# Performance work log

Measured on AMD Instinct MI355X. Metric: run time of the kernel, lower is better.

## Reference

```python
import jax, jax.numpy as jnp
import numpy as np

N = 100000      # nodes
E = 3200000     # edges (avg degree 32)
F_IN = 500      # PubMed node features
H = 16          # hidden
C = 3           # PubMed classes


def setup_inputs() -> dict:
    key = jax.random.key(0)
    k1, k2, k3, k4, k5, k6 = jax.random.split(key, 6)
    x = jax.random.normal(k1, (N, F_IN), dtype=jnp.float32)
    edge_index = jax.random.randint(k2, (2, E), 0, N, dtype=jnp.int32)
    # GCNConv weights (glorot-ish scale) and zero biases
    W1 = jax.random.normal(k3, (F_IN, H), dtype=jnp.float32) * np.float32(np.sqrt(2.0 / (F_IN + H)))
    b1 = jnp.zeros((H,), dtype=jnp.float32)
    W2 = jax.random.normal(k4, (H, C), dtype=jnp.float32) * np.float32(np.sqrt(2.0 / (H + C)))
    b2 = jnp.zeros((C,), dtype=jnp.float32)
    return {"x": x, "W1": W1, "b1": b1, "W2": W2, "b2": b2, "edge_index": edge_index}


def gcn_layer(x, W, b, src, dst, n):
    # GCNConv: linear transform, add self-loops, symmetric degree normalization, scatter-add
    h = x @ W                                   # [N, F_out]
    loop = jnp.arange(n, dtype=src.dtype)
    s = jnp.concatenate([src, loop])            # [E+N]
    d = jnp.concatenate([dst, loop])            # [E+N]
    deg = jax.ops.segment_sum(jnp.ones_like(d, dtype=h.dtype), d, num_segments=n)
    dinv = jax.lax.rsqrt(jnp.maximum(deg, 1.0))  # deg >= 1 due to self-loops
    norm = dinv[s] * dinv[d]                    # [E+N]
    out = jax.ops.segment_sum(h[s] * norm[:, None], d, num_segments=n)
    return out + b


def reference(x, W1, b1, W2, b2, edge_index):
    src, dst = edge_index[0], edge_index[1]
    h = gcn_layer(x, W1, b1, src, dst, N)
    h = jax.nn.relu(h)
    # F.dropout in eval mode (reference is deterministic) is identity
    out = gcn_layer(h, W2, b2, src, dst, N)
    return jax.nn.log_softmax(out, axis=1)
```

## Files before the change

### kernel.cpp

```cpp
#include <hip/hip_runtime.h>
#include <hip/hip_fp16.h>
#include <math.h>

#define N_NODES 100000
#define N_EDGES 3200000
#define F_INF   500
#define H_DIM   16
#define C_DIM   3

#define NB      782
#define CAP     4608
#define GPAD    16
#define EPB     16384
#define NBLK_PART ((N_EDGES + EPB - 1) / EPB)

#define OFF_GCUR  0
#define OFF_DINV  12512
#define OFF_PAIRS 112512
#define OFF_ROWS  3715968
#define OFF_H1H   3816064
#define OFF_H2H   4616064

typedef float        f32x4 __attribute__((ext_vector_type(4)));
typedef unsigned int u32x4 __attribute__((ext_vector_type(4)));
typedef unsigned int u32x2 __attribute__((ext_vector_type(2)));

template <typename T>
__device__ inline T ntload(const T* p) { return __builtin_nontemporal_load(p); }
template <typename T>
__device__ inline void ntstore(T* p, T v) { __builtin_nontemporal_store(v, p); }

__device__ inline float2 h2f(unsigned u) {
    __half2 h = *reinterpret_cast<__half2*>(&u);
    return __half22float2(h);
}
__device__ inline unsigned f2h(float a, float b) {
    __half2 h = __floats2half2_rn(a, b);
    return *reinterpret_cast<unsigned*>(&h);
}

__global__ void k_init(int* __restrict__ gcur) {
    int b = blockIdx.x * 256 + threadIdx.x;
    if (b < NB) gcur[b * GPAD] = b * CAP;
}

__global__ __launch_bounds__(512) void k_part(const int* __restrict__ src,
                                              const int* __restrict__ dst,
                                              int* __restrict__ gcur,
                                              unsigned int* __restrict__ pairs) {
    __shared__ unsigned sbuf[EPB];
    __shared__ int lcnt[NB];
    __shared__ int lbase[NB];
    __shared__ int lstart[NB];
    __shared__ int lrank[NB];
    __shared__ int wtot[8];
    int t = threadIdx.x;
    int wid = t >> 6, lane = t & 63;
    int e0 = blockIdx.x * EPB;
    for (int i = t; i < NB; i += 512) { lcnt[i] = 0; lrank[i] = 0; }
    __syncthreads();
    for (int i = t; i < EPB; i += 512) {
        int e = e0 + i;
        if (e < N_EDGES) atomicAdd(&lcnt[ntload(dst + e) >> 7], 1);
    }
    __syncthreads();
    for (int b = t; b < NB; b += 512) {
        int c = lcnt[b];
        lbase[b] = c ? atomicAdd(&gcur[b * GPAD], c) : 0;
    }
    {
        int b0 = wid * 128 + lane * 2;
        int c0 = (b0 < NB) ? lcnt[b0] : 0;
        int c1 = (b0 + 1 < NB) ? lcnt[b0 + 1] : 0;
        int s = c0 + c1;
        int inc = s;
        for (int o = 1; o < 64; o <<= 1) { int y = __shfl_up(inc, o); if (lane >= o) inc += y; }
        if (lane == 63) wtot[wid] = inc;
        int excl = inc - s;
        if (b0 < NB) lstart[b0] = excl;
        if (b0 + 1 < NB) lstart[b0 + 1] = excl + c0;
    }
    __syncthreads();
    if (t == 0) { int r = 0; for (int w = 0; w < 8; ++w) { int v = wtot[w]; wtot[w] = r; r += v; } }
    __syncthreads();
    {
        int b0 = wid * 128 + lane * 2;
        int add = wtot[wid];
        if (b0 < NB) lstart[b0] += add;
        if (b0 + 1 < NB) lstart[b0 + 1] += add;
    }
    __syncthreads();
    for (int i = t; i < EPB; i += 512) {
        int e = e0 + i;
        if (e < N_EDGES) {
            int d = ntload(dst + e);
            int b = d >> 7;
            int r = atomicAdd(&lrank[b], 1);
            sbuf[lstart[b] + r] = ((unsigned)ntload(src + e) << 7) | (unsigned)(d & 127);
        }
    }
    __syncthreads();
    for (int b = wid; b < NB; b += 8) {
        int c = lcnt[b], ls = lstart[b], gb = lbase[b];
        int lim = (b + 1) * CAP;
        for (int i = lane; i < c; i += 64) {
            int pos = gb + i;
            if (pos < lim)
                pairs[pos] = sbuf[ls + i];
        }
    }
}

__global__ __launch_bounds__(512) void k_sort(unsigned int* __restrict__ pairs,
                                              const int* __restrict__ gcur,
                                              float* __restrict__ dinv,
                                              int* __restrict__ rows) {
    __shared__ unsigned sbuf[CAP];
    __shared__ unsigned sout[CAP];
    __shared__ int cnt[128];
    __shared__ int start[128];
    __shared__ int rank[128];
    int b = blockIdx.x, t = threadIdx.x;
    if (t < 128) { cnt[t] = 0; rank[t] = 0; }
    __syncthreads();
    int base = b * CAP;
    int n = min(gcur[b * GPAD] - base, CAP);
    for (int i = t; i < n; i += 512) {
        unsigned p = ntload(pairs + base + i);
        sbuf[i] = p;
        atomicAdd(&cnt[p & 127], 1);
    }
    __syncthreads();
    if (t < 64) {
        int c0 = cnt[2 * t], c1 = cnt[2 * t + 1];
        int s = c0 + c1;
        int inc = s;
        for (int o = 1; o < 64; o <<= 1) { int y = __shfl_up(inc, o); if (t >= o) inc += y; }
        int excl = inc - s;
        start[2 * t] = excl;
        start[2 * t + 1] = excl + c0;
        rows[b * 128 + 2 * t]     = (excl << 16) | c0;
        rows[b * 128 + 2 * t + 1] = ((excl + c0) << 16) | c1;
    }
    if (t >= 64 && t < 192) {
        int l = t - 64;
        int v = b * 128 + l;
        if (v < N_NODES) dinv[v] = rsqrtf((float)(cnt[l] + 1));
    }
    __syncthreads();
    for (int i = t; i < n; i += 512) {
        unsigned p = sbuf[i];
        int k = p & 127;
        int r = atomicAdd(&rank[k], 1);
        sout[start[k] + r] = p;
    }
    __syncthreads();
    for (int i = t; i < n; i += 512) ntstore(pairs + base + i, sout[i]);
}

#define KTILE 16
#define KSTRIDE 17
#define GROWS 128
#define NFULL 31
#define KTAIL 4
#define NTILE 32
__global__ __launch_bounds__(128, 8) void k_gemm1(const float* __restrict__ x,
                                                  const float* __restrict__ W1,
                                                  const float* __restrict__ dinv,
                                                  unsigned int* __restrict__ h1h) {
    __shared__ float xs[GROWS * KSTRIDE];
    int t = threadIdx.x;
    int row0 = blockIdx.x * GROWS;
    int row = row0 + t;
    int cc = t & 3;
    int rr = t >> 2;
    float acc[16];
#pragma unroll
    for (int j = 0; j < 16; ++j) acc[j] = 0.f;
    f32x4 vreg[4];
#pragma unroll
    for (int s = 0; s < 4; ++s) {
        int gr = row0 + s * 32 + rr;
        if (gr < N_NODES)
            vreg[s] = ntload(reinterpret_cast<const f32x4*>(x + (size_t)gr * F_INF + cc * 4));
    }
#pragma unroll 1
    for (int tile = 0; tile < NTILE; ++tile) {
        int k0 = tile * KTILE;
        int nchunks = (tile < NFULL) ? 4 : 1;
        __syncthreads();
#pragma unroll
        for (int s = 0; s < 4; ++s) {
            int r = s * 32 + rr;
            if (cc < nchunks && row0 + r < N_NODES) {
                float* q = xs + r * KSTRIDE + cc * 4;
                q[0] = vreg[s].x; q[1] = vreg[s].y; q[2] = vreg[s].z; q[3] = vreg[s].w;
            }
        }
        __syncthreads();
        if (tile < NTILE - 1) {
            int nk0 = k0 + KTILE;
            int nnc = (tile + 1 < NFULL) ? 4 : 1;
#pragma unroll
            for (int s = 0; s < 4; ++s) {
                int gr = row0 + s * 32 + rr;
                if (cc < nnc && gr < N_NODES)
                    vreg[s] = ntload(reinterpret_cast<const f32x4*>(x + (size_t)gr * F_INF + nk0 + cc * 4));
            }
        }
        if (row < N_NODES) {
            const float* xrow = xs + t * KSTRIDE;
            const float* Wt = W1 + k0 * 16;
            if (tile < NFULL) {
#pragma unroll
                for (int kk = 0; kk < KTILE; ++kk) {
                    float xv = xrow[kk];
#pragma unroll
                    for (int j = 0; j < 16; ++j) acc[j] = fmaf(xv, Wt[kk * 16 + j], acc[j]);
                }
            } else {
#pragma unroll
                for (int kk = 0; kk < KTAIL; ++kk) {
                    float xv = xrow[kk];
#pragma unroll
                    for (int j = 0; j < 16; ++j) acc[j] = fmaf(xv, Wt[kk * 16 + j], acc[j]);
                }
            }
        }
    }
    if (row < N_NODES) {
        float dv = dinv[row];
        u32x4 o0, o1;
        o0.x = f2h(dv * acc[0],  dv * acc[1]);  o0.y = f2h(dv * acc[2],  dv * acc[3]);
        o0.z = f2h(dv * acc[4],  dv * acc[5]);  o0.w = f2h(dv * acc[6],  dv * acc[7]);
        o1.x = f2h(dv * acc[8],  dv * acc[9]);  o1.y = f2h(dv * acc[10], dv * acc[11]);
        o1.z = f2h(dv * acc[12], dv * acc[13]); o1.w = f2h(dv * acc[14], dv * acc[15]);
        u32x4* o = reinterpret_cast<u32x4*>(h1h + (size_t)row * 8);
        ntstore(o, o0);
        ntstore(o + 1, o1);
    }
}

__global__ __launch_bounds__(512) void k_agg1(const unsigned int* __restrict__ pairs,
                                              const int* __restrict__ rows,
                                              const float* __restrict__ dinv,
                                              const unsigned int* __restrict__ h1h,
                                              const float* __restrict__ b1,
                                              const float* __restrict__ W2,
                                              unsigned int* __restrict__ h2h) {
    int b = blockIdx.x, t = threadIdx.x;
    int q = t & 3;
    int l = t >> 2;
    int v = b * 128 + l;
    if (v >= N_NODES) return;
    int e = rows[b * 128 + l];
    int st = b * CAP + (e >> 16);
    int cnt = e & 0xffff;
    int qo = q * 2;
    float dv = dinv[v];
    float s0 = 0.f, s1 = 0.f, s2 = 0.f, s3 = 0.f;
    int i = 0;
    for (; i + 8 <= cnt; i += 8) {
        unsigned p[8];
#pragma unroll
        for (int u = 0; u < 8; ++u) p[u] = ntload(pairs + st + i + u);
        u32x2 A[8];
#pragma unroll
        for (int u = 0; u < 8; ++u)
            A[u] = *reinterpret_cast<const u32x2*>(h1h + (size_t)(p[u] >> 7) * 8 + qo);
#pragma unroll
        for (int u = 0; u < 8; ++u) {
            float2 f0 = h2f(A[u].x), f1 = h2f(A[u].y);
            s0 += f0.x; s1 += f0.y; s2 += f1.x; s3 += f1.y;
        }
    }
    for (; i < cnt; ++i) {
        unsigned p = ntload(pairs + st + i);
        u32x2 A = *reinterpret_cast<const u32x2*>(h1h + (size_t)(p >> 7) * 8 + qo);
        float2 f0 = h2f(A.x), f1 = h2f(A.y);
        s0 += f0.x; s1 += f0.y; s2 += f1.x; s3 += f1.y;
    }
    u32x2 S = *reinterpret_cast<const u32x2*>(h1h + (size_t)v * 8 + qo);
    float2 t0 = h2f(S.x), t1 = h2f(S.y);
    f32x4 bb = reinterpret_cast<const f32x4*>(b1)[q];
    float a0 = fmaxf(fmaf(dv, s0 + t0.x, bb.x), 0.f);
    float a1 = fmaxf(fmaf(dv, s1 + t0.y, bb.y), 0.f);
    float a2 = fmaxf(fmaf(dv, s2 + t1.x, bb.z), 0.f);
    float a3 = fmaxf(fmaf(dv, s3 + t1.y, bb.w), 0.f);
    const float* Wq = W2 + q * 4 * 3;
    float c0 = fmaf(a0, Wq[0], fmaf(a1, Wq[3], fmaf(a2, Wq[6],  a3 * Wq[9])));
    float c1 = fmaf(a0, Wq[1], fmaf(a1, Wq[4], fmaf(a2, Wq[7],  a3 * Wq[10])));
    float c2 = fmaf(a0, Wq[2], fmaf(a1, Wq[5], fmaf(a2, Wq[8],  a3 * Wq[11])));
    c0 += __shfl_xor(c0, 1); c0 += __shfl_xor(c0, 2);
    c1 += __shfl_xor(c1, 1); c1 += __shfl_xor(c1, 2);
    c2 += __shfl_xor(c2, 1); c2 += __shfl_xor(c2, 2);
    if (q == 0) {
        u32x2 o;
        o.x = f2h(dv * c0, dv * c1);
        o.y = f2h(dv * c2, 0.f);
        ntstore(reinterpret_cast<u32x2*>(h2h) + v, o);
    }
}

__global__ __launch_bounds__(256) void k_agg2(const unsigned int* __restrict__ pairs,
                                              const int* __restrict__ rows,
                                              const float* __restrict__ dinv,
                                              const unsigned int* __restrict__ h2h,
                                              const float* __restrict__ b2,
                                              float* __restrict__ out) {
    int b = blockIdx.x, t = threadIdx.x;
    int half = t & 1;
    int l = t >> 1;
    int v = b * 128 + l;
    if (v >= N_NODES) return;
    int e = rows[b * 128 + l];
    int st = b * CAP + (e >> 16);
    int cnt = e & 0xffff;
    const u32x2* h2v = reinterpret_cast<const u32x2*>(h2h);
    float c0 = 0.f, c1 = 0.f, c2 = 0.f;
    int i = half;
    for (; i + 6 < cnt; i += 8) {
        unsigned p0 = ntload(pairs + st + i);
        unsigned p1 = ntload(pairs + st + i + 2);
        unsigned p2 = ntload(pairs + st + i + 4);
        unsigned p3 = ntload(pairs + st + i + 6);
        u32x2 A = h2v[p0 >> 7];
        u32x2 B = h2v[p1 >> 7];
        u32x2 C = h2v[p2 >> 7];
        u32x2 D = h2v[p3 >> 7];
        float2 f01, f2_;
        f01 = h2f(A.x); f2_ = h2f(A.y); c0 += f01.x; c1 += f01.y; c2 += f2_.x;
        f01 = h2f(B.x); f2_ = h2f(B.y); c0 += f01.x; c1 += f01.y; c2 += f2_.x;
        f01 = h2f(C.x); f2_ = h2f(C.y); c0 += f01.x; c1 += f01.y; c2 += f2_.x;
        f01 = h2f(D.x); f2_ = h2f(D.y); c0 += f01.x; c1 += f01.y; c2 += f2_.x;
    }
    for (; i < cnt; i += 2) {
        unsigned p = ntload(pairs + st + i);
        u32x2 A = h2v[p >> 7];
        float2 f01 = h2f(A.x), f2_ = h2f(A.y);
        c0 += f01.x; c1 += f01.y; c2 += f2_.x;
    }
    c0 += __shfl_xor(c0, 1);
    c1 += __shfl_xor(c1, 1);
    c2 += __shfl_xor(c2, 1);
    if (half == 0) {
        float dv = dinv[v];
        u32x2 hv = h2v[v];
        float2 f01 = h2f(hv.x), f2_ = h2f(hv.y);
        float z0 = fmaf(dv, c0 + f01.x, b2[0]);
        float z1 = fmaf(dv, c1 + f01.y, b2[1]);
        float z2 = fmaf(dv, c2 + f2_.x, b2[2]);
        float mx = fmaxf(z0, fmaxf(z1, z2));
        float lse = logf(expf(z0 - mx) + expf(z1 - mx) + expf(z2 - mx));
        out[v * 3 + 0] = z0 - mx - lse;
        out[v * 3 + 1] = z1 - mx - lse;
        out[v * 3 + 2] = z2 - mx - lse;
    }
}

extern "C" void kernel_launch(void* const* d_in, const int* in_sizes, int n_in,
                              void* d_out, int out_size, void* d_ws, size_t ws_size,
                              hipStream_t stream) {
    (void)in_sizes; (void)n_in; (void)out_size; (void)ws_size;
    const float* x  = (const float*)d_in[0];
    const float* W1 = (const float*)d_in[1];
    const float* b1 = (const float*)d_in[2];
    const float* W2 = (const float*)d_in[3];
    const float* b2 = (const float*)d_in[4];
    const int*   ei = (const int*)d_in[5];
    const int* src = ei;
    const int* dst = ei + N_EDGES;
    float* out = (float*)d_out;

    int* ws = (int*)d_ws;
    int*          gcur  = ws + OFF_GCUR;
    float*        dinv  = (float*)(ws + OFF_DINV);
    unsigned int* pairs = (unsigned int*)(ws + OFF_PAIRS);
    int*          rows  = ws + OFF_ROWS;
    unsigned int* h1h   = (unsigned int*)(ws + OFF_H1H);
    unsigned int* h2h   = (unsigned int*)(ws + OFF_H2H);

    k_init <<<(NB + 255) / 256, 256, 0, stream>>>(gcur);
    k_part <<<NBLK_PART, 512, 0, stream>>>(src, dst, gcur, pairs);
    k_sort <<<NB, 512, 0, stream>>>(pairs, gcur, dinv, rows);
    k_gemm1<<<NB, GROWS, 0, stream>>>(x, W1, dinv, h1h);
    k_agg1 <<<NB, 512, 0, stream>>>(pairs, rows, dinv, h1h, b1, W2, h2h);
    k_agg2 <<<NB, 256, 0, stream>>>(pairs, rows, dinv, h2h, b2, out);
}
```

Before: 524.9 us.

## Split each GEMM1 row across four threads and stage W1 in LDS

```diff
diff --git a/kernel.cpp b/kernel.cpp
--- a/kernel.cpp
+++ b/kernel.cpp
@@ -159,85 +159,85 @@
 }
 
 #define KTILE 16
-#define KSTRIDE 17
+#define KSTRIDE 20
 #define GROWS 128
 #define NFULL 31
-#define KTAIL 4
 #define NTILE 32
-__global__ __launch_bounds__(128, 8) void k_gemm1(const float* __restrict__ x,
+__global__ __launch_bounds__(512, 6) void k_gemm1(const float* __restrict__ x,
                                                   const float* __restrict__ W1,
                                                   const float* __restrict__ dinv,
                                                   unsigned int* __restrict__ h1h) {
     __shared__ float xs[GROWS * KSTRIDE];
+    __shared__ float wlds[F_INF * 16];
     int t = threadIdx.x;
     int row0 = blockIdx.x * GROWS;
-    int row = row0 + t;
-    int cc = t & 3;
-    int rr = t >> 2;
-    float acc[16];
-#pragma unroll
-    for (int j = 0; j < 16; ++j) acc[j] = 0.f;
-    f32x4 vreg[4];
-#pragma unroll
-    for (int s = 0; s < 4; ++s) {
-        int gr = row0 + s * 32 + rr;
-        if (gr < N_NODES)
-            vreg[s] = ntload(reinterpret_cast<const f32x4*>(x + (size_t)gr * F_INF + cc * 4));
-    }
+    int q = t & 3;
+    int r = t >> 2;
+    int row = row0 + r;
+    bool rowok = row < N_NODES;
+
+    {
+        const f32x4* Wg = reinterpret_cast<const f32x4*>(W1);
+        f32x4* Wl = reinterpret_cast<f32x4*>(wlds);
+        for (int i = t; i < F_INF * 4; i += 512) Wl[i] = ntload(Wg + i);
+    }
+
+    float acc[4] = {0.f, 0.f, 0.f, 0.f};
+    f32x4 vreg;
+    if (rowok)
+        vreg = ntload(reinterpret_cast<const f32x4*>(x + (size_t)row * F_INF + q * 4));
+
 #pragma unroll 1
     for (int tile = 0; tile < NTILE; ++tile) {
         int k0 = tile * KTILE;
-        int nchunks = (tile < NFULL) ? 4 : 1;
         __syncthreads();
-#pragma unroll
-        for (int s = 0; s < 4; ++s) {
-            int r = s * 32 + rr;
-            if (cc < nchunks && row0 + r < N_NODES) {
-                float* q = xs + r * KSTRIDE + cc * 4;
-                q[0] = vreg[s].x; q[1] = vreg[s].y; q[2] = vreg[s].z; q[3] = vreg[s].w;
-            }
+        if (rowok && (tile < NFULL || q == 0)) {
+            float* p = xs + r * KSTRIDE + q * 4;
+            p[0] = vreg.x; p[1] = vreg.y; p[2] = vreg.z; p[3] = vreg.w;
         }
         __syncthreads();
         if (tile < NTILE - 1) {
             int nk0 = k0 + KTILE;
-            int nnc = (tile + 1 < NFULL) ? 4 : 1;
-#pragma unroll
-            for (int s = 0; s < 4; ++s) {
-                int gr = row0 + s * 32 + rr;
-                if (cc < nnc && gr < N_NODES)
-                    vreg[s] = ntload(reinterpret_cast<const f32x4*>(x + (size_t)gr * F_INF + nk0 + cc * 4));
-            }
-        }
-        if (row < N_NODES) {
-            const float* xrow = xs + t * KSTRIDE;
-            const float* Wt = W1 + k0 * 16;
+            if (rowok && (tile + 1 < NFULL || q == 0))
+                vreg = ntload(reinterpret_cast<const f32x4*>(x + (size_t)row * F_INF + nk0 + q * 4));
+        }
+        if (rowok) {
+            const float* xrow = xs + r * KSTRIDE;
+            const float* wq = wlds + k0 * 16 + q * 4;
             if (tile < NFULL) {
 #pragma unroll
-                for (int kk = 0; kk < KTILE; ++kk) {
-                    float xv = xrow[kk];
-#pragma unroll
-                    for (int j = 0; j < 16; ++j) acc[j] = fmaf(xv, Wt[kk * 16 + j], acc[j]);
+                for (int g = 0; g < 4; ++g) {
+                    f32x4 xv = *reinterpret_cast<const f32x4*>(xrow + g * 4);
+#pragma unroll
+                    for (int kk = 0; kk < 4; ++kk) {
+                        f32x4 wv = *reinterpret_cast<const f32x4*>(wq + (g * 4 + kk) * 16);
+                        float xvk = xv[kk];
+                        acc[0] = fmaf(xvk, wv.x, acc[0]);
+                        acc[1] = fmaf(xvk, wv.y, acc[1]);
+                        acc[2] = fmaf(xvk, wv.z, acc[2]);
+                        acc[3] = fmaf(xvk, wv.w, acc[3]);
+                    }
                 }
             } else {
-#pragma unroll
-                for (int kk = 0; kk < KTAIL; ++kk) {
-                    float xv = xrow[kk];
-#pragma unroll
-                    for (int j = 0; j < 16; ++j) acc[j] = fmaf(xv, Wt[kk * 16 + j], acc[j]);
+                f32x4 xv = *reinterpret_cast<const f32x4*>(xrow);
+#pragma unroll
+                for (int kk = 0; kk < 4; ++kk) {
+                    f32x4 wv = *reinterpret_cast<const f32x4*>(wq + kk * 16);
+                    float xvk = xv[kk];
+                    acc[0] = fmaf(xvk, wv.x, acc[0]);
+                    acc[1] = fmaf(xvk, wv.y, acc[1]);
+                    acc[2] = fmaf(xvk, wv.z, acc[2]);
+                    acc[3] = fmaf(xvk, wv.w, acc[3]);
                 }
             }
         }
     }
-    if (row < N_NODES) {
+    if (rowok) {
         float dv = dinv[row];
-        u32x4 o0, o1;
-        o0.x = f2h(dv * acc[0],  dv * acc[1]);  o0.y = f2h(dv * acc[2],  dv * acc[3]);
-        o0.z = f2h(dv * acc[4],  dv * acc[5]);  o0.w = f2h(dv * acc[6],  dv * acc[7]);
-        o1.x = f2h(dv * acc[8],  dv * acc[9]);  o1.y = f2h(dv * acc[10], dv * acc[11]);
-        o1.z = f2h(dv * acc[12], dv * acc[13]); o1.w = f2h(dv * acc[14], dv * acc[15]);
-        u32x4* o = reinterpret_cast<u32x4*>(h1h + (size_t)row * 8);
-        ntstore(o, o0);
-        ntstore(o + 1, o1);
+        u32x2 o;
+        o.x = f2h(dv * acc[0], dv * acc[1]);
+        o.y = f2h(dv * acc[2], dv * acc[3]);
+        ntstore(reinterpret_cast<u32x2*>(h1h + (size_t)row * 8 + q * 2), o);
     }
 }
 
@@ -383,7 +383,7 @@
     k_init <<<(NB + 255) / 256, 256, 0, stream>>>(gcur);
     k_part <<<NBLK_PART, 512, 0, stream>>>(src, dst, gcur, pairs);
     k_sort <<<NB, 512, 0, stream>>>(pairs, gcur, dinv, rows);
-    k_gemm1<<<NB, GROWS, 0, stream>>>(x, W1, dinv, h1h);
+    k_gemm1<<<NB, 512, 0, stream>>>(x, W1, dinv, h1h);
     k_agg1 <<<NB, 512, 0, stream>>>(pairs, rows, dinv, h1h, b1, W2, h2h);
     k_agg2 <<<NB, 256, 0, stream>>>(pairs, rows, dinv, h2h, b2, out);
 }
```

After: 489.5 us. 6.7% less time.

## Split GEMM1 K dimension across four waves with 64-wide tiles and smem reduction

Applied to the files above, without the earlier changes.

```diff
diff --git a/kernel.cpp b/kernel.cpp
--- a/kernel.cpp
+++ b/kernel.cpp
@@ -158,25 +158,29 @@
     for (int i = t; i < n; i += 512) ntstore(pairs + base + i, sout[i]);
 }
 
-#define KTILE 16
-#define KSTRIDE 17
-#define GROWS 128
-#define NFULL 31
-#define KTAIL 4
-#define NTILE 32
-__global__ __launch_bounds__(128, 8) void k_gemm1(const float* __restrict__ x,
+#define GK_ROWS 128
+#define GK_STRIDE 68
+#define GK_ROUNDS 8
+__global__ __launch_bounds__(512, 6) void k_gemm1(const float* __restrict__ x,
                                                   const float* __restrict__ W1,
                                                   const float* __restrict__ dinv,
                                                   unsigned int* __restrict__ h1h) {
-    __shared__ float xs[GROWS * KSTRIDE];
+    __shared__ float smem[GK_ROWS * GK_STRIDE];
     int t = threadIdx.x;
-    int row0 = blockIdx.x * GROWS;
-    int row = row0 + t;
-    int cc = t & 3;
-    int rr = t >> 2;
+    int row0 = blockIdx.x * GK_ROWS;
+    int cc = t & 15;
+    int rr = t >> 4;
+    int lane = t & 63;
+    int wid  = t >> 6;
+    int g    = wid & 3;
+    int crow = (wid >> 2) * 64 + lane;
+    int grow = row0 + crow;
+    bool rowok = grow < N_NODES;
+
     float acc[16];
 #pragma unroll
     for (int j = 0; j < 16; ++j) acc[j] = 0.f;
+
     f32x4 vreg[4];
 #pragma unroll
     for (int s = 0; s < 4; ++s) {
@@ -184,60 +188,90 @@
         if (gr < N_NODES)
             vreg[s] = ntload(reinterpret_cast<const f32x4*>(x + (size_t)gr * F_INF + cc * 4));
     }
+
 #pragma unroll 1
-    for (int tile = 0; tile < NTILE; ++tile) {
-        int k0 = tile * KTILE;
-        int nchunks = (tile < NFULL) ? 4 : 1;
+    for (int rd = 0; rd < GK_ROUNDS; ++rd) {
+        int k0 = rd * 64;
+        int kw = (rd < GK_ROUNDS - 1) ? 64 : (F_INF - 64 * (GK_ROUNDS - 1));
         __syncthreads();
-#pragma unroll
-        for (int s = 0; s < 4; ++s) {
-            int r = s * 32 + rr;
-            if (cc < nchunks && row0 + r < N_NODES) {
-                float* q = xs + r * KSTRIDE + cc * 4;
-                q[0] = vreg[s].x; q[1] = vreg[s].y; q[2] = vreg[s].z; q[3] = vreg[s].w;
+        if (cc * 4 < kw) {
+#pragma unroll
+            for (int s = 0; s < 4; ++s) {
+                int r = s * 32 + rr;
+                if (row0 + r < N_NODES) {
+                    float* p = smem + r * GK_STRIDE + cc * 4;
+                    p[0] = vreg[s].x; p[1] = vreg[s].y; p[2] = vreg[s].z; p[3] = vreg[s].w;
+                }
             }
         }
         __syncthreads();
-        if (tile < NTILE - 1) {
-            int nk0 = k0 + KTILE;
-            int nnc = (tile + 1 < NFULL) ? 4 : 1;
-#pragma unroll
-            for (int s = 0; s < 4; ++s) {
-                int gr = row0 + s * 32 + rr;
-                if (cc < nnc && gr < N_NODES)
-                    vreg[s] = ntload(reinterpret_cast<const f32x4*>(x + (size_t)gr * F_INF + nk0 + cc * 4));
+        if (rd < GK_ROUNDS - 1) {
+            int nk0 = k0 + 64;
+            int nkw = (rd + 1 < GK_ROUNDS - 1) ? 64 : (F_INF - 64 * (GK_ROUNDS - 1));
+            if (cc * 4 < nkw) {
+#pragma unroll
+                for (int s = 0; s < 4; ++s) {
+                    int gr = row0 + s * 32 + rr;
+                    if (gr < N_NODES)
+                        vreg[s] = ntload(reinterpret_cast<const f32x4*>(x + (size_t)gr * F_INF + nk0 + cc * 4));
+                }
             }
         }
-        if (row < N_NODES) {
-            const float* xrow = xs + t * KSTRIDE;
-            const float* Wt = W1 + k0 * 16;
-            if (tile < NFULL) {
-#pragma unroll
-                for (int kk = 0; kk < KTILE; ++kk) {
-                    float xv = xrow[kk];
-#pragma unroll
-                    for (int j = 0; j < 16; ++j) acc[j] = fmaf(xv, Wt[kk * 16 + j], acc[j]);
+        int klen = kw - g * 16; if (klen > 16) klen = 16;
+        if (klen > 0 && rowok) {
+            const float* xr = smem + crow * GK_STRIDE + g * 16;
+            const float* Wu = W1 + (k0 + g * 16) * 16;
+            if (klen == 16) {
+#pragma unroll
+                for (int c4 = 0; c4 < 4; ++c4) {
+                    f32x4 xv = *reinterpret_cast<const f32x4*>(xr + c4 * 4);
+#pragma unroll
+                    for (int kk = 0; kk < 4; ++kk) {
+                        float xvk = xv[kk];
+                        const float* wk = Wu + (c4 * 4 + kk) * 16;
+#pragma unroll
+                        for (int j = 0; j < 16; ++j) acc[j] = fmaf(xvk, wk[j], acc[j]);
+                    }
                 }
             } else {
-#pragma unroll
-                for (int kk = 0; kk < KTAIL; ++kk) {
-                    float xv = xrow[kk];
-#pragma unroll
-                    for (int j = 0; j < 16; ++j) acc[j] = fmaf(xv, Wt[kk * 16 + j], acc[j]);
+                f32x4 xv = *reinterpret_cast<const f32x4*>(xr);
+#pragma unroll
+                for (int kk = 0; kk < 4; ++kk) {
+                    float xvk = xv[kk];
+                    const float* wk = Wu + kk * 16;
+#pragma unroll
+                    for (int j = 0; j < 16; ++j) acc[j] = fmaf(xvk, wk[j], acc[j]);
                 }
             }
         }
     }
-    if (row < N_NODES) {
-        float dv = dinv[row];
-        u32x4 o0, o1;
-        o0.x = f2h(dv * acc[0],  dv * acc[1]);  o0.y = f2h(dv * acc[2],  dv * acc[3]);
-        o0.z = f2h(dv * acc[4],  dv * acc[5]);  o0.w = f2h(dv * acc[6],  dv * acc[7]);
-        o1.x = f2h(dv * acc[8],  dv * acc[9]);  o1.y = f2h(dv * acc[10], dv * acc[11]);
-        o1.z = f2h(dv * acc[12], dv * acc[13]); o1.w = f2h(dv * acc[14], dv * acc[15]);
-        u32x4* o = reinterpret_cast<u32x4*>(h1h + (size_t)row * 8);
-        ntstore(o, o0);
-        ntstore(o + 1, o1);
+    __syncthreads();
+    {
+        float* red = smem + crow * GK_STRIDE + g * 16;
+#pragma unroll
+        for (int j = 0; j < 16; j += 4) {
+            f32x4 v; v.x = acc[j]; v.y = acc[j + 1]; v.z = acc[j + 2]; v.w = acc[j + 3];
+            *reinterpret_cast<f32x4*>(red + j) = v;
+        }
+    }
+    __syncthreads();
+    {
+        int fr = t >> 2, q = t & 3;
+        int v = row0 + fr;
+        if (v < N_NODES) {
+            const float* rb = smem + fr * GK_STRIDE + q * 4;
+            f32x4 s0 = *reinterpret_cast<const f32x4*>(rb);
+            f32x4 s1 = *reinterpret_cast<const f32x4*>(rb + 16);
+            f32x4 s2 = *reinterpret_cast<const f32x4*>(rb + 32);
+            f32x4 s3 = *reinterpret_cast<const f32x4*>(rb + 48);
+            float dv = dinv[v];
+            float r0 = dv * (s0.x + s1.x + s2.x + s3.x);
+            float r1 = dv * (s0.y + s1.y + s2.y + s3.y);
+            float r2 = dv * (s0.z + s1.z + s2.z + s3.z);
+            float r3 = dv * (s0.w + s1.w + s2.w + s3.w);
+            u32x2 o; o.x = f2h(r0, r1); o.y = f2h(r2, r3);
+            ntstore(reinterpret_cast<u32x2*>(h1h + (size_t)v * 8 + q * 2), o);
+        }
     }
 }
 
@@ -383,7 +417,7 @@
     k_init <<<(NB + 255) / 256, 256, 0, stream>>>(gcur);
     k_part <<<NBLK_PART, 512, 0, stream>>>(src, dst, gcur, pairs);
     k_sort <<<NB, 512, 0, stream>>>(pairs, gcur, dinv, rows);
-    k_gemm1<<<NB, GROWS, 0, stream>>>(x, W1, dinv, h1h);
+    k_gemm1<<<NB, 512, 0, stream>>>(x, W1, dinv, h1h);
     k_agg1 <<<NB, 512, 0, stream>>>(pairs, rows, dinv, h1h, b1, W2, h2h);
     k_agg2 <<<NB, 256, 0, stream>>>(pairs, rows, dinv, h2h, b2, out);
 }
```

New measurement: 644.4 us. 1.23x slower.
